# Kernel tuning notes

Hardware: AMD Instinct MI355X
Metric: run time of the kernel (lower is better)

The kernel has to match this reference:

```python
import jax, jax.numpy as jnp
import numpy as np

D_M, D_K, D_V, HEADS = 1024, 64, 64, 16
B, S = 2, 2048


def setup_inputs() -> dict:
    key = jax.random.key(0)
    ks = jax.random.split(key, 5)
    x = jax.random.normal(ks[0], (B, S, D_M), dtype=jnp.float32)
    # per-head projection weights (original deep-copies one rand init per head;
    # we give each head independent weights, matching the per-head param structure)
    Wk = jax.random.uniform(ks[1], (HEADS, D_M, D_K), dtype=jnp.float32)
    Wq = jax.random.uniform(ks[2], (HEADS, D_M, D_K), dtype=jnp.float32)
    Wv = jax.random.uniform(ks[3], (HEADS, D_M, D_V), dtype=jnp.float32)
    Wo = jax.random.uniform(ks[4], (HEADS * D_V, D_M), dtype=jnp.float32)
    return {"x": x, "Wk": Wk, "Wq": Wq, "Wv": Wv, "Wo": Wo}


def reference(x, Wk, Wq, Wv, Wo):
    # per-head QKV projections, batched over heads: [B,H,S,d]
    q = jnp.einsum("bsm,hmk->bhsk", x, Wq)
    k = jnp.einsum("bsm,hmk->bhsk", x, Wk)
    v = jnp.einsum("bsm,hmv->bhsv", x, Wv)
    scale = 1.0 / jnp.sqrt(jnp.asarray(q.shape[-1], dtype=q.dtype))
    scores = jnp.einsum("bhsk,bhtk->bhst", q, k) * scale  # [B,H,S,S]
    attn = jax.nn.softmax(scores, axis=-1)
    ctx = jnp.einsum("bhst,bhtv->bhsv", attn, v)  # [B,H,S,d_v]
    # concat heads -> [B,S,H*d_v], then output projection
    ctx = jnp.transpose(ctx, (0, 2, 1, 3)).reshape(x.shape[0], x.shape[1], -1)
    return jnp.einsum("bsc,cm->bsm", ctx, Wo)
```

## Files before the change

### kernel.cpp

```cpp
#include <hip/hip_runtime.h>
#include <hip/hip_bf16.h>
#include <stdint.h>

#define DM   1024
#define DKV  64
#define HEADS 16
#define BATCH 2
#define SEQ  2048
#define BS   (BATCH*SEQ)
#define BHD  (BATCH*HEADS)

typedef __attribute__((ext_vector_type(8))) short bf16x8;
typedef __attribute__((ext_vector_type(4))) short bf16x4;
typedef __attribute__((ext_vector_type(4))) float f32x4;

__device__ inline unsigned fb(float f) { union { float f; unsigned u; } v; v.f = f; return v.u; }

__device__ inline unsigned short bf16_rtn(float f) {
  unsigned u = fb(f);
  unsigned r = u + 0x7fffu + ((u >> 16) & 1u);
  return (unsigned short)(r >> 16);
}
__device__ inline float bf16_to_f(unsigned short h) {
  union { unsigned u; float f; } v; v.u = ((unsigned)h) << 16; return v.f;
}
__device__ inline void split_bf16(float x, unsigned short& hi, unsigned short& lo) {
  hi = bf16_rtn(x);
  lo = bf16_rtn(x - bf16_to_f(hi));
}
__device__ inline unsigned pack2_bf16(float lo_elem, float hi_elem) {
  return __builtin_amdgcn_perm(fb(hi_elem) + 0x8000u, fb(lo_elem) + 0x8000u, 0x07060302u);
}

__device__ inline float fast_exp2(float x) {
#if __has_builtin(__builtin_amdgcn_exp2f)
  return __builtin_amdgcn_exp2f(x);
#else
  return exp2f(x);
#endif
}

__device__ inline f32x4 mfma16x16x16_bf16(bf16x4 a, bf16x4 b, f32x4 c) {
#if __has_builtin(__builtin_amdgcn_mfma_f32_16x16x16bf16_1k)
  return __builtin_amdgcn_mfma_f32_16x16x16bf16_1k(a, b, c, 0, 0, 0);
#else
  asm volatile("v_mfma_f32_16x16x16_bf16 %0, %1, %2, %0" : "+v"(c) : "v"(a), "v"(b));
  return c;
#endif
}

__device__ inline void stage16(const unsigned short* g, unsigned short* lds_base, int lane) {
#if __has_builtin(__builtin_amdgcn_global_load_lds)
  __builtin_amdgcn_global_load_lds((__attribute__((address_space(1))) void*)(g),
                                   (__attribute__((address_space(3))) void*)(lds_base),
                                   16, 0, 0);
#else
  *(bf16x8*)(lds_base + lane * 8) = *(const bf16x8*)g;
#endif
}

__device__ inline int swz(int row, int chunk) {
  return row * 64 + (((chunk ^ (row & 7)) & 7) << 3);
}

__global__ void cvt_x_split(const float* __restrict__ x,
                            unsigned short* __restrict__ xh, unsigned short* __restrict__ xl) {
  int i = (blockIdx.x * 256 + threadIdx.x) * 8;
  bf16x8 oh, ol;
  #pragma unroll
  for (int j = 0; j < 8; ++j) {
    unsigned short hi, lo;
    split_bf16(x[i + j], hi, lo);
    oh[j] = (short)hi; ol[j] = (short)lo;
  }
  *(bf16x8*)(xh + i) = oh;
  *(bf16x8*)(xl + i) = ol;
}

__global__ void pack_qkv_split(const float* __restrict__ Wq, const float* __restrict__ Wk,
                               const float* __restrict__ Wv,
                               unsigned short* __restrict__ Wh, unsigned short* __restrict__ Wl) {
  __shared__ float tile[64][65];
  int bid = blockIdx.x;
  int p = bid >> 8, h = (bid >> 4) & 15, mt = bid & 15;
  const float* W = (p == 0) ? Wq : (p == 1) ? Wk : Wv;
  const float* src = W + (size_t)h * (DM * DKV);
  int t = threadIdx.x;
  int m0 = mt * 64;
  #pragma unroll
  for (int pass = 0; pass < 16; ++pass) {
    int row = pass * 4 + (t >> 6), col = t & 63;
    tile[row][col] = src[(size_t)(m0 + row) * DKV + col];
  }
  __syncthreads();
  int cbase = p * 1024 + h * 64;
  #pragma unroll
  for (int pass = 0; pass < 16; ++pass) {
    int krow = pass * 4 + (t >> 6), mcol = t & 63;
    unsigned short hi, lo;
    split_bf16(tile[mcol][krow], hi, lo);
    size_t idx = (size_t)(cbase + krow) * DM + m0 + mcol;
    Wh[idx] = hi; Wl[idx] = lo;
  }
}

__global__ void pack_wo(const float* __restrict__ Wo, unsigned short* __restrict__ WoT) {
  __shared__ float tile[64][65];
  int ib = blockIdx.x >> 4, jb = blockIdx.x & 15;
  int t = threadIdx.x;
  #pragma unroll
  for (int pass = 0; pass < 16; ++pass) {
    int row = pass * 4 + (t >> 6), col = t & 63;
    tile[row][col] = Wo[(size_t)(ib * 64 + row) * DM + jb * 64 + col];
  }
  __syncthreads();
  #pragma unroll
  for (int pass = 0; pass < 16; ++pass) {
    int a = pass * 4 + (t >> 6), b = t & 63;
    WoT[(size_t)(jb * 64 + a) * DM + ib * 64 + b] = bf16_rtn(tile[b][a]);
  }
}

__global__ __launch_bounds__(256, 2)
void gemm_qk(const unsigned short* __restrict__ Ah, const unsigned short* __restrict__ Al,
             const unsigned short* __restrict__ Bh, const unsigned short* __restrict__ Bl,
             unsigned short* __restrict__ Qh, unsigned short* __restrict__ Ql,
             unsigned short* __restrict__ Kh, unsigned short* __restrict__ Kl) {
  __shared__ unsigned short AsH[128 * 64], AsL[128 * 64];
  __shared__ unsigned short BsH[128 * 64], BsL[128 * 64];
  const int tid = threadIdx.x;
  const int w = tid >> 6, lane = tid & 63;
  const int quad = lane >> 4, l16 = lane & 15;
  const int wm = w >> 1, wn = w & 1;
  const int bn = blockIdx.x, bm = blockIdx.y;

  f32x4 acc[4][4];
  #pragma unroll
  for (int i = 0; i < 4; ++i)
    #pragma unroll
    for (int j = 0; j < 4; ++j) acc[i][j] = (f32x4){0.f, 0.f, 0.f, 0.f};

  const int r8 = lane >> 3, c8 = lane & 7;
  const int cs = c8 ^ r8;
  const size_t offA = (size_t)(bm * 128 + w * 32 + r8) * DM + cs * 8;
  const size_t offB = (size_t)(bn * 128 + w * 32 + r8) * DM + cs * 8;

  for (int kk = 0; kk < DM / 64; ++kk) {
    #pragma unroll
    for (int ps = 0; ps < 4; ++ps) {
      unsigned short* dA = AsH + (w * 32 + ps * 8) * 64;
      unsigned short* dAl = AsL + (w * 32 + ps * 8) * 64;
      unsigned short* dB = BsH + (w * 32 + ps * 8) * 64;
      unsigned short* dBl = BsL + (w * 32 + ps * 8) * 64;
      stage16(Ah + offA + kk * 64 + ps * 8 * DM, dA,  lane);
      stage16(Al + offA + kk * 64 + ps * 8 * DM, dAl, lane);
      stage16(Bh + offB + kk * 64 + ps * 8 * DM, dB,  lane);
      stage16(Bl + offB + kk * 64 + ps * 8 * DM, dBl, lane);
    }
    asm volatile("s_waitcnt vmcnt(0)" ::: "memory");
    __syncthreads();
    #pragma unroll
    for (int ks = 0; ks < 2; ++ks) {
      bf16x8 afh[4], afl[4], bfh[4], bfl[4];
      #pragma unroll
      for (int mt = 0; mt < 4; ++mt) {
        int row = wm * 64 + mt * 16 + l16;
        int ad = row * 64 + ((((ks * 4 + quad) ^ (row & 7)) & 7) << 3);
        afh[mt] = *(const bf16x8*)(AsH + ad);
        afl[mt] = *(const bf16x8*)(AsL + ad);
      }
      #pragma unroll
      for (int nt = 0; nt < 4; ++nt) {
        int row = wn * 64 + nt * 16 + l16;
        int ad = row * 64 + ((((ks * 4 + quad) ^ (row & 7)) & 7) << 3);
        bfh[nt] = *(const bf16x8*)(BsH + ad);
        bfl[nt] = *(const bf16x8*)(BsL + ad);
      }
      #pragma unroll
      for (int mt = 0; mt < 4; ++mt)
        #pragma unroll
        for (int nt = 0; nt < 4; ++nt) {
          acc[mt][nt] = __builtin_amdgcn_mfma_f32_16x16x32_bf16(afh[mt], bfh[nt], acc[mt][nt], 0, 0, 0);
          acc[mt][nt] = __builtin_amdgcn_mfma_f32_16x16x32_bf16(afh[mt], bfl[nt], acc[mt][nt], 0, 0, 0);
          acc[mt][nt] = __builtin_amdgcn_mfma_f32_16x16x32_bf16(afl[mt], bfh[nt], acc[mt][nt], 0, 0, 0);
        }
    }
    __syncthreads();
  }

  const float SCL = 0.18033688011112042f;
  #pragma unroll
  for (int mt = 0; mt < 4; ++mt) {
    int m_g = bm * 128 + wm * 64 + mt * 16 + quad * 4;
    #pragma unroll
    for (int nt = 0; nt < 4; ++nt) {
      int n_g = bn * 128 + wn * 64 + nt * 16 + l16;
      int p = n_g >> 10, h = (n_g >> 6) & 15, k = n_g & 63;
      #pragma unroll
      for (int r = 0; r < 4; ++r) {
        int row = m_g + r;
        int b = row >> 11, s = row & 2047;
        int bh = b * HEADS + h;
        float v = acc[mt][nt][r];
        size_t idx = ((size_t)(bh * SEQ + s)) * DKV + k;
        unsigned short hi, lo;
        if (p == 0) {
          split_bf16(v * SCL, hi, lo);
          Qh[idx] = hi; Ql[idx] = lo;
        } else {
          split_bf16(v, hi, lo);
          Kh[idx] = hi; Kl[idx] = lo;
        }
      }
    }
  }
}

__global__ __launch_bounds__(256, 2)
void gemm_v(const unsigned short* __restrict__ A, const unsigned short* __restrict__ Bt,
            unsigned short* __restrict__ Vt) {
  __shared__ unsigned short As[64 * 64];
  __shared__ unsigned short Bs[128 * 64];
  const int tid = threadIdx.x;
  const int w = tid >> 6, lane = tid & 63;
  const int quad = lane >> 4, l16 = lane & 15;
  const int wm = w >> 1, wn = w & 1;
  const int bn = blockIdx.x, bm = blockIdx.y;

  f32x4 acc[2][4];
  #pragma unroll
  for (int i = 0; i < 2; ++i)
    #pragma unroll
    for (int j = 0; j < 4; ++j) acc[i][j] = (f32x4){0.f, 0.f, 0.f, 0.f};

  const int r8 = lane >> 3, c8 = lane & 7;
  const int cs = c8 ^ r8;
  const size_t offA = (size_t)(bm * 64 + w * 16 + r8) * DM + cs * 8;
  const size_t offB = (size_t)(bn * 128 + w * 32 + r8) * DM + cs * 8;

  for (int kk = 0; kk < DM / 64; ++kk) {
    #pragma unroll
    for (int ps = 0; ps < 2; ++ps)
      stage16(A + offA + kk * 64 + ps * 8 * DM, As + (w * 16 + ps * 8) * 64, lane);
    #pragma unroll
    for (int ps = 0; ps < 4; ++ps)
      stage16(Bt + offB + kk * 64 + ps * 8 * DM, Bs + (w * 32 + ps * 8) * 64, lane);
    asm volatile("s_waitcnt vmcnt(0)" ::: "memory");
    __syncthreads();
    #pragma unroll
    for (int ks = 0; ks < 2; ++ks) {
      bf16x8 af[2], bfr[4];
      #pragma unroll
      for (int mt = 0; mt < 2; ++mt) {
        int row = wm * 32 + mt * 16 + l16;
        af[mt] = *(const bf16x8*)(As + row * 64 + ((((ks * 4 + quad) ^ (row & 7)) & 7) << 3));
      }
      #pragma unroll
      for (int nt = 0; nt < 4; ++nt) {
        int row = wn * 64 + nt * 16 + l16;
        bfr[nt] = *(const bf16x8*)(Bs + row * 64 + ((((ks * 4 + quad) ^ (row & 7)) & 7) << 3));
      }
      #pragma unroll
      for (int mt = 0; mt < 2; ++mt)
        #pragma unroll
        for (int nt = 0; nt < 4; ++nt)
          acc[mt][nt] = __builtin_amdgcn_mfma_f32_16x16x32_bf16(af[mt], bfr[nt], acc[mt][nt], 0, 0, 0);
    }
    __syncthreads();
  }

  #pragma unroll
  for (int mt = 0; mt < 2; ++mt) {
    int m_g = bm * 64 + wm * 32 + mt * 16 + quad * 4;
    #pragma unroll
    for (int nt = 0; nt < 4; ++nt) {
      int n_g = bn * 128 + wn * 64 + nt * 16 + l16;
      int h = n_g >> 6, k = n_g & 63;
      #pragma unroll
      for (int r = 0; r < 4; ++r) {
        int row = m_g + r;
        int b = row >> 11, s = row & 2047;
        int bh = b * HEADS + h;
        Vt[((size_t)(bh * DKV + k)) * SEQ + s] = bf16_rtn(acc[mt][nt][r]);
      }
    }
  }
}

__global__ __launch_bounds__(256, 2)
void flash(const unsigned short* __restrict__ Qh, const unsigned short* __restrict__ Ql,
           const unsigned short* __restrict__ Kh, const unsigned short* __restrict__ Kl,
           const unsigned short* __restrict__ Vt, unsigned short* __restrict__ ctx) {
  __shared__ unsigned short KtH[2][64 * 64], KtL[2][64 * 64], Vts[2][64 * 64];
  const int tid = threadIdx.x;
  const int w = tid >> 6, lane = tid & 63, quad = lane >> 4, l16 = lane & 15;
  const int bh = blockIdx.x;
  const int q0 = blockIdx.y * 128;

  bf16x8 qfh[2][2], qfl[2][2];
  #pragma unroll
  for (int qt = 0; qt < 2; ++qt) {
    int qrow = q0 + w * 32 + qt * 16 + l16;
    size_t base = ((size_t)(bh * SEQ + qrow)) * DKV + quad * 8;
    qfh[qt][0] = *(const bf16x8*)(Qh + base);
    qfh[qt][1] = *(const bf16x8*)(Qh + base + 32);
    qfl[qt][0] = *(const bf16x8*)(Ql + base);
    qfl[qt][1] = *(const bf16x8*)(Ql + base + 32);
  }

  float m_run[2] = {-1e30f, -1e30f};
  float l_run[2] = {0.f, 0.f};
  f32x4 acc[2][4];
  #pragma unroll
  for (int qt = 0; qt < 2; ++qt)
    #pragma unroll
    for (int vt = 0; vt < 4; ++vt) acc[qt][vt] = (f32x4){0.f, 0.f, 0.f, 0.f};

  const int srow = w * 16 + (lane >> 3);
  const int csrc = (lane & 7) ^ (lane >> 3);
  const unsigned short* kh_src = Kh + ((size_t)(bh * SEQ) + srow) * DKV + csrc * 8;
  const unsigned short* kl_src = Kl + ((size_t)(bh * SEQ) + srow) * DKV + csrc * 8;
  const unsigned short* v_src  = Vt + ((size_t)(bh * DKV) + srow) * SEQ + csrc * 8;

  #define STAGE_K(buf, kt0)                                                     \
    do {                                                                        \
      unsigned short* dH = &KtH[buf][(w * 16) * 64];                            \
      unsigned short* dL = &KtL[buf][(w * 16) * 64];                            \
      stage16(kh_src + (size_t)(kt0) * 64 * DKV,           dH,       lane);     \
      stage16(kh_src + (size_t)(kt0) * 64 * DKV + 8 * DKV, dH + 512, lane);     \
      stage16(kl_src + (size_t)(kt0) * 64 * DKV,           dL,       lane);     \
      stage16(kl_src + (size_t)(kt0) * 64 * DKV + 8 * DKV, dL + 512, lane);     \
    } while (0)
  #define STAGE_V(buf, kt0)                                                     \
    do {                                                                        \
      unsigned short* dV = &Vts[buf][(w * 16) * 64];                            \
      stage16(v_src + (kt0) * 64,           dV,       lane);                    \
      stage16(v_src + (kt0) * 64 + 8 * SEQ, dV + 512, lane);                    \
    } while (0)

  #define QK_HALF(STV, KHP, KLP, MT0)                                           \
    _Pragma("unroll")                                                           \
    for (int mt = (MT0); mt < (MT0) + 2; ++mt) {                                \
      int rowA = mt * 16 + l16;                                                 \
      bf16x8 kah0 = *(const bf16x8*)((KHP) + swz(rowA, quad));                  \
      bf16x8 kah1 = *(const bf16x8*)((KHP) + swz(rowA, quad + 4));              \
      bf16x8 kal0 = *(const bf16x8*)((KLP) + swz(rowA, quad));                  \
      bf16x8 kal1 = *(const bf16x8*)((KLP) + swz(rowA, quad + 4));              \
      _Pragma("unroll")                                                         \
      for (int qt = 0; qt < 2; ++qt) {                                          \
        f32x4 c = (f32x4){0.f, 0.f, 0.f, 0.f};                                  \
        c = __builtin_amdgcn_mfma_f32_16x16x32_bf16(kah0, qfh[qt][0], c, 0, 0, 0); \
        c = __builtin_amdgcn_mfma_f32_16x16x32_bf16(kah1, qfh[qt][1], c, 0, 0, 0); \
        c = __builtin_amdgcn_mfma_f32_16x16x32_bf16(kah0, qfl[qt][0], c, 0, 0, 0); \
        c = __builtin_amdgcn_mfma_f32_16x16x32_bf16(kah1, qfl[qt][1], c, 0, 0, 0); \
        c = __builtin_amdgcn_mfma_f32_16x16x32_bf16(kal0, qfh[qt][0], c, 0, 0, 0); \
        c = __builtin_amdgcn_mfma_f32_16x16x32_bf16(kal1, qfh[qt][1], c, 0, 0, 0); \
        (STV)[mt][qt] = c;                                                      \
      }                                                                         \
    }

  #define SM_QT(QT)                                                             \
    {                                                                           \
      float cm = -1e30f;                                                        \
      _Pragma("unroll")                                                         \
      for (int mt = 0; mt < 4; ++mt)                                            \
        _Pragma("unroll")                                                       \
        for (int r = 0; r < 4; ++r) cm = fmaxf(cm, st[mt][QT][r]);              \
      cm = fmaxf(cm, __shfl_xor(cm, 16));                                       \
      cm = fmaxf(cm, __shfl_xor(cm, 32));                                       \
      float mn = fmaxf(cm, m_run[QT]);                                          \
      float ssum = 0.f;                                                         \
      _Pragma("unroll")                                                         \
      for (int mt = 0; mt < 4; ++mt) {                                          \
        float p0 = fast_exp2(st[mt][QT][0] - mn);                               \
        float p1 = fast_exp2(st[mt][QT][1] - mn);                               \
        float p2 = fast_exp2(st[mt][QT][2] - mn);                               \
        float p3 = fast_exp2(st[mt][QT][3] - mn);                               \
        ssum += (p0 + p1) + (p2 + p3);                                          \
        union { bf16x4 v; unsigned u2[2]; } pk;                                 \
        pk.u2[0] = pack2_bf16(p0, p1);                                          \
        pk.u2[1] = pack2_bf16(p2, p3);                                          \
        pb[QT][mt] = pk.v;                                                      \
      }                                                                         \
      ssum += __shfl_xor(ssum, 16);                                             \
      ssum += __shfl_xor(ssum, 32);                                             \
      float alpha = fast_exp2(m_run[QT] - mn);                                  \
      m_run[QT] = mn;                                                           \
      l_run[QT] = l_run[QT] * alpha + ssum;                                     \
      _Pragma("unroll")                                                         \
      for (int vt = 0; vt < 4; ++vt) acc[QT][vt] = acc[QT][vt] * alpha;         \
    }

  #define PV_ALL(VSP)                                                           \
    _Pragma("unroll")                                                           \
    for (int vt = 0; vt < 4; ++vt)                                              \
      _Pragma("unroll")                                                         \
      for (int mt = 0; mt < 4; ++mt) {                                          \
        int row = vt * 16 + l16;                                                \
        int addr = row * 64 + ((((mt * 2 + (quad >> 1)) ^ (row & 7)) & 7) << 3) + (quad & 1) * 4; \
        bf16x4 va = *(const bf16x4*)((VSP) + addr);                             \
        _Pragma("unroll")                                                       \
        for (int qt = 0; qt < 2; ++qt)                                          \
          acc[qt][vt] = mfma16x16x16_bf16(va, pb[qt][mt], acc[qt][vt]);         \
      }

  STAGE_K(0, 0);
  STAGE_V(0, 0);
  STAGE_K(1, 1);
  asm volatile("s_waitcnt vmcnt(0)" ::: "memory");
  __syncthreads();

  f32x4 st[4][2];
  QK_HALF(st, KtH[0], KtL[0], 0);
  QK_HALF(st, KtH[0], KtL[0], 2);

  #pragma unroll 2
  for (int t = 0; t < SEQ / 64 - 1; ++t) {
    const int cb = t & 1, nb = (t + 1) & 1;
    if (t + 2 < SEQ / 64) STAGE_K(cb, t + 2);
    STAGE_V(nb, t + 1);

    const unsigned short* kHn = KtH[nb];
    const unsigned short* kLn = KtL[nb];
    const unsigned short* vS  = Vts[cb];

    bf16x4 pb[2][4];
    f32x4 stn[4][2];
    SM_QT(0);
    QK_HALF(stn, kHn, kLn, 0);
    SM_QT(1);
    QK_HALF(stn, kHn, kLn, 2);
    PV_ALL(vS);

    #pragma unroll
    for (int mt = 0; mt < 4; ++mt)
      #pragma unroll
      for (int qt = 0; qt < 2; ++qt) st[mt][qt] = stn[mt][qt];

    asm volatile("s_waitcnt vmcnt(0)" ::: "memory");
    __syncthreads();
  }

  {
    bf16x4 pb[2][4];
    SM_QT(0);
    SM_QT(1);
    PV_ALL(Vts[(SEQ / 64 - 1) & 1]);
  }
  #undef STAGE_K
  #undef STAGE_V
  #undef QK_HALF
  #undef SM_QT
  #undef PV_ALL

  int h = bh & 15, b = bh >> 4;
  #pragma unroll
  for (int qt = 0; qt < 2; ++qt) {
    float inv = 1.0f / l_run[qt];
    int bs = b * SEQ + q0 + w * 32 + qt * 16 + l16;
    #pragma unroll
    for (int vt = 0; vt < 4; ++vt) {
      union { bf16x4 v; unsigned u2[2]; } pk;
      pk.u2[0] = pack2_bf16(acc[qt][vt][0] * inv, acc[qt][vt][1] * inv);
      pk.u2[1] = pack2_bf16(acc[qt][vt][2] * inv, acc[qt][vt][3] * inv);
      *(bf16x4*)(ctx + (size_t)bs * DM + h * 64 + vt * 16 + quad * 4) = pk.v;
    }
  }
}

__global__ __launch_bounds__(256, 2)
void gemm_out(const unsigned short* __restrict__ A, const unsigned short* __restrict__ Bt,
              float* __restrict__ out) {
  __shared__ unsigned short As[64 * 64];
  __shared__ unsigned short Bs[128 * 64];
  const int tid = threadIdx.x;
  const int w = tid >> 6, lane = tid & 63;
  const int quad = lane >> 4, l16 = lane & 15;
  const int wm = w >> 1, wn = w & 1;
  const int bn = blockIdx.x, bm = blockIdx.y;

  f32x4 acc[2][4];
  #pragma unroll
  for (int i = 0; i < 2; ++i)
    #pragma unroll
    for (int j = 0; j < 4; ++j) acc[i][j] = (f32x4){0.f, 0.f, 0.f, 0.f};

  const int r8 = lane >> 3, c8 = lane & 7;
  const int cs = c8 ^ r8;
  const size_t offA = (size_t)(bm * 64 + w * 16 + r8) * DM + cs * 8;
  const size_t offB = (size_t)(bn * 128 + w * 32 + r8) * DM + cs * 8;

  for (int kk = 0; kk < DM / 64; ++kk) {
    #pragma unroll
    for (int ps = 0; ps < 2; ++ps)
      stage16(A + offA + kk * 64 + ps * 8 * DM, As + (w * 16 + ps * 8) * 64, lane);
    #pragma unroll
    for (int ps = 0; ps < 4; ++ps)
      stage16(Bt + offB + kk * 64 + ps * 8 * DM, Bs + (w * 32 + ps * 8) * 64, lane);
    asm volatile("s_waitcnt vmcnt(0)" ::: "memory");
    __syncthreads();
    #pragma unroll
    for (int ks = 0; ks < 2; ++ks) {
      bf16x8 af[2], bfr[4];
      #pragma unroll
      for (int mt = 0; mt < 2; ++mt) {
        int row = wm * 32 + mt * 16 + l16;
        af[mt] = *(const bf16x8*)(As + row * 64 + ((((ks * 4 + quad) ^ (row & 7)) & 7) << 3));
      }
      #pragma unroll
      for (int nt = 0; nt < 4; ++nt) {
        int row = wn * 64 + nt * 16 + l16;
        bfr[nt] = *(const bf16x8*)(Bs + row * 64 + ((((ks * 4 + quad) ^ (row & 7)) & 7) << 3));
      }
      #pragma unroll
      for (int mt = 0; mt < 2; ++mt)
        #pragma unroll
        for (int nt = 0; nt < 4; ++nt)
          acc[mt][nt] = __builtin_amdgcn_mfma_f32_16x16x32_bf16(af[mt], bfr[nt], acc[mt][nt], 0, 0, 0);
    }
    __syncthreads();
  }

  #pragma unroll
  for (int mt = 0; mt < 2; ++mt) {
    int m_g = bm * 64 + wm * 32 + mt * 16 + quad * 4;
    #pragma unroll
    for (int nt = 0; nt < 4; ++nt) {
      int n_g = bn * 128 + wn * 64 + nt * 16 + l16;
      #pragma unroll
      for (int r = 0; r < 4; ++r)
        out[(size_t)(m_g + r) * DM + n_g] = acc[mt][nt][r];
    }
  }
}

extern "C" void kernel_launch(void* const* d_in, const int* in_sizes, int n_in,
                              void* d_out, int out_size, void* d_ws, size_t ws_size,
                              hipStream_t stream) {
  const float* x  = (const float*)d_in[0];
  const float* Wk = (const float*)d_in[1];
  const float* Wq = (const float*)d_in[2];
  const float* Wv = (const float*)d_in[3];
  const float* Wo = (const float*)d_in[4];
  float* out = (float*)d_out;

  unsigned short* xh  = (unsigned short*)d_ws;
  unsigned short* xl  = xh  + (size_t)BS * DM;
  unsigned short* Wh  = xl  + (size_t)BS * DM;
  unsigned short* Wl  = Wh  + (size_t)3 * DM * DM;
  unsigned short* WoT = Wl  + (size_t)3 * DM * DM;
  unsigned short* Qh  = WoT + (size_t)DM * DM;
  unsigned short* Ql  = Qh  + (size_t)BHD * SEQ * DKV;
  unsigned short* Kh  = Ql  + (size_t)BHD * SEQ * DKV;
  unsigned short* Kl  = Kh  + (size_t)BHD * SEQ * DKV;
  unsigned short* Vtb = Kl  + (size_t)BHD * SEQ * DKV;
  unsigned short* ctx = Vtb + (size_t)BHD * SEQ * DKV;

  cvt_x_split<<<(BS * DM) / (256 * 8), 256, 0, stream>>>(x, xh, xl);
  pack_qkv_split<<<3 * 16 * 16, 256, 0, stream>>>(Wq, Wk, Wv, Wh, Wl);
  pack_wo<<<16 * 16, 256, 0, stream>>>(Wo, WoT);
  gemm_qk<<<dim3(16, 32), 256, 0, stream>>>(xh, xl, Wh, Wl, Qh, Ql, Kh, Kl);
  gemm_v<<<dim3(8, 64), 256, 0, stream>>>(xh, Wh + (size_t)2048 * DM, Vtb);
  flash<<<dim3(BHD, SEQ / 128), 256, 0, stream>>>(Qh, Ql, Kh, Kl, Vtb, ctx);
  gemm_out<<<dim3(8, 64), 256, 0, stream>>>(ctx, WoT, out);
}
```

Baseline: 251.7 us.

## Merge QK and V projection kernels, add lazy softmax rescale and MFMA priority

The separate QK and V projection GEMMs become one launch, with blocks 0–511 doing the split-precision QK work and blocks 512–1023 doing V from a shared LDS buffer, removing a launch and letting the two workloads overlap. In the flash kernel, the running max and rescale are only updated when some lane's local max exceeds the running max by more than 8. The cross-lane row-sum reduction moves to the epilogue. s_setprio is raised around the MFMA sections. The lazy threshold relies on exp2 values up to 2^8 staying safe in bf16/fp32, and the merged kernel now reserves the larger LDS footprint for every block.

```diff
diff --git a/kernel.cpp b/kernel.cpp
--- a/kernel.cpp
+++ b/kernel.cpp
@@ -122,166 +122,162 @@
 }
 
 __global__ __launch_bounds__(256, 2)
-void gemm_qk(const unsigned short* __restrict__ Ah, const unsigned short* __restrict__ Al,
-             const unsigned short* __restrict__ Bh, const unsigned short* __restrict__ Bl,
-             unsigned short* __restrict__ Qh, unsigned short* __restrict__ Ql,
-             unsigned short* __restrict__ Kh, unsigned short* __restrict__ Kl) {
-  __shared__ unsigned short AsH[128 * 64], AsL[128 * 64];
-  __shared__ unsigned short BsH[128 * 64], BsL[128 * 64];
+void gemm_qkv(const unsigned short* __restrict__ Ah, const unsigned short* __restrict__ Al,
+              const unsigned short* __restrict__ Bh, const unsigned short* __restrict__ Bl,
+              unsigned short* __restrict__ Qh, unsigned short* __restrict__ Ql,
+              unsigned short* __restrict__ Kh, unsigned short* __restrict__ Kl,
+              unsigned short* __restrict__ Vt) {
+  __shared__ unsigned short smem[32768];
   const int tid = threadIdx.x;
   const int w = tid >> 6, lane = tid & 63;
   const int quad = lane >> 4, l16 = lane & 15;
   const int wm = w >> 1, wn = w & 1;
-  const int bn = blockIdx.x, bm = blockIdx.y;
-
-  f32x4 acc[4][4];
-  #pragma unroll
-  for (int i = 0; i < 4; ++i)
-    #pragma unroll
-    for (int j = 0; j < 4; ++j) acc[i][j] = (f32x4){0.f, 0.f, 0.f, 0.f};
-
+  const int bid = blockIdx.x;
   const int r8 = lane >> 3, c8 = lane & 7;
   const int cs = c8 ^ r8;
-  const size_t offA = (size_t)(bm * 128 + w * 32 + r8) * DM + cs * 8;
-  const size_t offB = (size_t)(bn * 128 + w * 32 + r8) * DM + cs * 8;
-
-  for (int kk = 0; kk < DM / 64; ++kk) {
-    #pragma unroll
-    for (int ps = 0; ps < 4; ++ps) {
-      unsigned short* dA = AsH + (w * 32 + ps * 8) * 64;
-      unsigned short* dAl = AsL + (w * 32 + ps * 8) * 64;
-      unsigned short* dB = BsH + (w * 32 + ps * 8) * 64;
-      unsigned short* dBl = BsL + (w * 32 + ps * 8) * 64;
-      stage16(Ah + offA + kk * 64 + ps * 8 * DM, dA,  lane);
-      stage16(Al + offA + kk * 64 + ps * 8 * DM, dAl, lane);
-      stage16(Bh + offB + kk * 64 + ps * 8 * DM, dB,  lane);
-      stage16(Bl + offB + kk * 64 + ps * 8 * DM, dBl, lane);
-    }
-    asm volatile("s_waitcnt vmcnt(0)" ::: "memory");
-    __syncthreads();
-    #pragma unroll
-    for (int ks = 0; ks < 2; ++ks) {
-      bf16x8 afh[4], afl[4], bfh[4], bfl[4];
-      #pragma unroll
-      for (int mt = 0; mt < 4; ++mt) {
-        int row = wm * 64 + mt * 16 + l16;
-        int ad = row * 64 + ((((ks * 4 + quad) ^ (row & 7)) & 7) << 3);
-        afh[mt] = *(const bf16x8*)(AsH + ad);
-        afl[mt] = *(const bf16x8*)(AsL + ad);
-      }
+
+  if (bid < 512) {
+    unsigned short* AsH = smem;
+    unsigned short* AsL = smem + 8192;
+    unsigned short* BsH = smem + 16384;
+    unsigned short* BsL = smem + 24576;
+    const int bn = bid & 15, bm = bid >> 4;
+
+    f32x4 acc[4][4];
+    #pragma unroll
+    for (int i = 0; i < 4; ++i)
+      #pragma unroll
+      for (int j = 0; j < 4; ++j) acc[i][j] = (f32x4){0.f, 0.f, 0.f, 0.f};
+
+    const size_t offA = (size_t)(bm * 128 + w * 32 + r8) * DM + cs * 8;
+    const size_t offB = (size_t)(bn * 128 + w * 32 + r8) * DM + cs * 8;
+
+    for (int kk = 0; kk < DM / 64; ++kk) {
+      #pragma unroll
+      for (int ps = 0; ps < 4; ++ps) {
+        stage16(Ah + offA + kk * 64 + ps * 8 * DM, AsH + (w * 32 + ps * 8) * 64, lane);
+        stage16(Al + offA + kk * 64 + ps * 8 * DM, AsL + (w * 32 + ps * 8) * 64, lane);
+        stage16(Bh + offB + kk * 64 + ps * 8 * DM, BsH + (w * 32 + ps * 8) * 64, lane);
+        stage16(Bl + offB + kk * 64 + ps * 8 * DM, BsL + (w * 32 + ps * 8) * 64, lane);
+      }
+      asm volatile("s_waitcnt vmcnt(0)" ::: "memory");
+      __syncthreads();
+      #pragma unroll
+      for (int ks = 0; ks < 2; ++ks) {
+        bf16x8 afh[4], afl[4], bfh[4], bfl[4];
+        #pragma unroll
+        for (int mt = 0; mt < 4; ++mt) {
+          int row = wm * 64 + mt * 16 + l16;
+          int ad = row * 64 + ((((ks * 4 + quad) ^ (row & 7)) & 7) << 3);
+          afh[mt] = *(const bf16x8*)(AsH + ad);
+          afl[mt] = *(const bf16x8*)(AsL + ad);
+        }
+        #pragma unroll
+        for (int nt = 0; nt < 4; ++nt) {
+          int row = wn * 64 + nt * 16 + l16;
+          int ad = row * 64 + ((((ks * 4 + quad) ^ (row & 7)) & 7) << 3);
+          bfh[nt] = *(const bf16x8*)(BsH + ad);
+          bfl[nt] = *(const bf16x8*)(BsL + ad);
+        }
+        #pragma unroll
+        for (int mt = 0; mt < 4; ++mt)
+          #pragma unroll
+          for (int nt = 0; nt < 4; ++nt) {
+            acc[mt][nt] = __builtin_amdgcn_mfma_f32_16x16x32_bf16(afh[mt], bfh[nt], acc[mt][nt], 0, 0, 0);
+            acc[mt][nt] = __builtin_amdgcn_mfma_f32_16x16x32_bf16(afh[mt], bfl[nt], acc[mt][nt], 0, 0, 0);
+            acc[mt][nt] = __builtin_amdgcn_mfma_f32_16x16x32_bf16(afl[mt], bfh[nt], acc[mt][nt], 0, 0, 0);
+          }
+      }
+      __syncthreads();
+    }
+
+    const float SCL = 0.18033688011112042f;
+    #pragma unroll
+    for (int mt = 0; mt < 4; ++mt) {
+      int m_g = bm * 128 + wm * 64 + mt * 16 + quad * 4;
       #pragma unroll
       for (int nt = 0; nt < 4; ++nt) {
-        int row = wn * 64 + nt * 16 + l16;
-        int ad = row * 64 + ((((ks * 4 + quad) ^ (row & 7)) & 7) << 3);
-        bfh[nt] = *(const bf16x8*)(BsH + ad);
-        bfl[nt] = *(const bf16x8*)(BsL + ad);
-      }
-      #pragma unroll
-      for (int mt = 0; mt < 4; ++mt)
+        int n_g = bn * 128 + wn * 64 + nt * 16 + l16;
+        int p = n_g >> 10, h = (n_g >> 6) & 15, k = n_g & 63;
+        #pragma unroll
+        for (int r = 0; r < 4; ++r) {
+          int row = m_g + r;
+          int b = row >> 11, s = row & 2047;
+          int bh = b * HEADS + h;
+          float v = acc[mt][nt][r];
+          size_t idx = ((size_t)(bh * SEQ + s)) * DKV + k;
+          unsigned short hi, lo;
+          if (p == 0) {
+            split_bf16(v * SCL, hi, lo);
+            Qh[idx] = hi; Ql[idx] = lo;
+          } else {
+            split_bf16(v, hi, lo);
+            Kh[idx] = hi; Kl[idx] = lo;
+          }
+        }
+      }
+    }
+  } else {
+    unsigned short* As = smem;
+    unsigned short* Bs = smem + 4096;
+    const int vid = bid - 512;
+    const int bn = vid & 7, bm = vid >> 3;
+    const unsigned short* Bt = Bh + (size_t)2048 * DM;
+
+    f32x4 acc[2][4];
+    #pragma unroll
+    for (int i = 0; i < 2; ++i)
+      #pragma unroll
+      for (int j = 0; j < 4; ++j) acc[i][j] = (f32x4){0.f, 0.f, 0.f, 0.f};
+
+    const size_t offA = (size_t)(bm * 64 + w * 16 + r8) * DM + cs * 8;
+    const size_t offB = (size_t)(bn * 128 + w * 32 + r8) * DM + cs * 8;
+
+    for (int kk = 0; kk < DM / 64; ++kk) {
+      #pragma unroll
+      for (int ps = 0; ps < 2; ++ps)
+        stage16(Ah + offA + kk * 64 + ps * 8 * DM, As + (w * 16 + ps * 8) * 64, lane);
+      #pragma unroll
+      for (int ps = 0; ps < 4; ++ps)
+        stage16(Bt + offB + kk * 64 + ps * 8 * DM, Bs + (w * 32 + ps * 8) * 64, lane);
+      asm volatile("s_waitcnt vmcnt(0)" ::: "memory");
+      __syncthreads();
+      #pragma unroll
+      for (int ks = 0; ks < 2; ++ks) {
+        bf16x8 af[2], bfr[4];
+        #pragma unroll
+        for (int mt = 0; mt < 2; ++mt) {
+          int row = wm * 32 + mt * 16 + l16;
+          af[mt] = *(const bf16x8*)(As + row * 64 + ((((ks * 4 + quad) ^ (row & 7)) & 7) << 3));
+        }
         #pragma unroll
         for (int nt = 0; nt < 4; ++nt) {
-          acc[mt][nt] = __builtin_amdgcn_mfma_f32_16x16x32_bf16(afh[mt], bfh[nt], acc[mt][nt], 0, 0, 0);
-          acc[mt][nt] = __builtin_amdgcn_mfma_f32_16x16x32_bf16(afh[mt], bfl[nt], acc[mt][nt], 0, 0, 0);
-          acc[mt][nt] = __builtin_amdgcn_mfma_f32_16x16x32_bf16(afl[mt], bfh[nt], acc[mt][nt], 0, 0, 0);
+          int row = wn * 64 + nt * 16 + l16;
+          bfr[nt] = *(const bf16x8*)(Bs + row * 64 + ((((ks * 4 + quad) ^ (row & 7)) & 7) << 3));
         }
-    }
-    __syncthreads();
-  }
-
-  const float SCL = 0.18033688011112042f;
-  #pragma unroll
-  for (int mt = 0; mt < 4; ++mt) {
-    int m_g = bm * 128 + wm * 64 + mt * 16 + quad * 4;
-    #pragma unroll
-    for (int nt = 0; nt < 4; ++nt) {
-      int n_g = bn * 128 + wn * 64 + nt * 16 + l16;
-      int p = n_g >> 10, h = (n_g >> 6) & 15, k = n_g & 63;
-      #pragma unroll
-      for (int r = 0; r < 4; ++r) {
-        int row = m_g + r;
-        int b = row >> 11, s = row & 2047;
-        int bh = b * HEADS + h;
-        float v = acc[mt][nt][r];
-        size_t idx = ((size_t)(bh * SEQ + s)) * DKV + k;
-        unsigned short hi, lo;
-        if (p == 0) {
-          split_bf16(v * SCL, hi, lo);
-          Qh[idx] = hi; Ql[idx] = lo;
-        } else {
-          split_bf16(v, hi, lo);
-          Kh[idx] = hi; Kl[idx] = lo;
+        #pragma unroll
+        for (int mt = 0; mt < 2; ++mt)
+          #pragma unroll
+          for (int nt = 0; nt < 4; ++nt)
+            acc[mt][nt] = __builtin_amdgcn_mfma_f32_16x16x32_bf16(af[mt], bfr[nt], acc[mt][nt], 0, 0, 0);
+      }
+      __syncthreads();
+    }
+
+    #pragma unroll
+    for (int mt = 0; mt < 2; ++mt) {
+      int m_g = bm * 64 + wm * 32 + mt * 16 + quad * 4;
+      #pragma unroll
+      for (int nt = 0; nt < 4; ++nt) {
+        int n_g = bn * 128 + wn * 64 + nt * 16 + l16;
+        int h = n_g >> 6, k = n_g & 63;
+        #pragma unroll
+        for (int r = 0; r < 4; ++r) {
+          int row = m_g + r;
+          int b = row >> 11, s = row & 2047;
+          int bh = b * HEADS + h;
+          Vt[((size_t)(bh * DKV + k)) * SEQ + s] = bf16_rtn(acc[mt][nt][r]);
         }
-      }
-    }
-  }
-}
-
-__global__ __launch_bounds__(256, 2)
-void gemm_v(const unsigned short* __restrict__ A, const unsigned short* __restrict__ Bt,
-            unsigned short* __restrict__ Vt) {
-  __shared__ unsigned short As[64 * 64];
-  __shared__ unsigned short Bs[128 * 64];
-  const int tid = threadIdx.x;
-  const int w = tid >> 6, lane = tid & 63;
-  const int quad = lane >> 4, l16 = lane & 15;
-  const int wm = w >> 1, wn = w & 1;
-  const int bn = blockIdx.x, bm = blockIdx.y;
-
-  f32x4 acc[2][4];
-  #pragma unroll
-  for (int i = 0; i < 2; ++i)
-    #pragma unroll
-    for (int j = 0; j < 4; ++j) acc[i][j] = (f32x4){0.f, 0.f, 0.f, 0.f};
-
-  const int r8 = lane >> 3, c8 = lane & 7;
-  const int cs = c8 ^ r8;
-  const size_t offA = (size_t)(bm * 64 + w * 16 + r8) * DM + cs * 8;
-  const size_t offB = (size_t)(bn * 128 + w * 32 + r8) * DM + cs * 8;
-
-  for (int kk = 0; kk < DM / 64; ++kk) {
-    #pragma unroll
-    for (int ps = 0; ps < 2; ++ps)
-      stage16(A + offA + kk * 64 + ps * 8 * DM, As + (w * 16 + ps * 8) * 64, lane);
-    #pragma unroll
-    for (int ps = 0; ps < 4; ++ps)
-      stage16(Bt + offB + kk * 64 + ps * 8 * DM, Bs + (w * 32 + ps * 8) * 64, lane);
-    asm volatile("s_waitcnt vmcnt(0)" ::: "memory");
-    __syncthreads();
-    #pragma unroll
-    for (int ks = 0; ks < 2; ++ks) {
-      bf16x8 af[2], bfr[4];
-      #pragma unroll
-      for (int mt = 0; mt < 2; ++mt) {
-        int row = wm * 32 + mt * 16 + l16;
-        af[mt] = *(const bf16x8*)(As + row * 64 + ((((ks * 4 + quad) ^ (row & 7)) & 7) << 3));
-      }
-      #pragma unroll
-      for (int nt = 0; nt < 4; ++nt) {
-        int row = wn * 64 + nt * 16 + l16;
-        bfr[nt] = *(const bf16x8*)(Bs + row * 64 + ((((ks * 4 + quad) ^ (row & 7)) & 7) << 3));
-      }
-      #pragma unroll
-      for (int mt = 0; mt < 2; ++mt)
-        #pragma unroll
-        for (int nt = 0; nt < 4; ++nt)
-          acc[mt][nt] = __builtin_amdgcn_mfma_f32_16x16x32_bf16(af[mt], bfr[nt], acc[mt][nt], 0, 0, 0);
-    }
-    __syncthreads();
-  }
-
-  #pragma unroll
-  for (int mt = 0; mt < 2; ++mt) {
-    int m_g = bm * 64 + wm * 32 + mt * 16 + quad * 4;
-    #pragma unroll
-    for (int nt = 0; nt < 4; ++nt) {
-      int n_g = bn * 128 + wn * 64 + nt * 16 + l16;
-      int h = n_g >> 6, k = n_g & 63;
-      #pragma unroll
-      for (int r = 0; r < 4; ++r) {
-        int row = m_g + r;
-        int b = row >> 11, s = row & 2047;
-        int bh = b * HEADS + h;
-        Vt[((size_t)(bh * DKV + k)) * SEQ + s] = bf16_rtn(acc[mt][nt][r]);
       }
     }
   }
@@ -366,9 +362,17 @@
       for (int mt = 0; mt < 4; ++mt)                                            \
         _Pragma("unroll")                                                       \
         for (int r = 0; r < 4; ++r) cm = fmaxf(cm, st[mt][QT][r]);              \
-      cm = fmaxf(cm, __shfl_xor(cm, 16));                                       \
-      cm = fmaxf(cm, __shfl_xor(cm, 32));                                       \
-      float mn = fmaxf(cm, m_run[QT]);                                          \
+      if (!__all(cm <= m_run[QT] + 8.0f)) {                                     \
+        cm = fmaxf(cm, __shfl_xor(cm, 16));                                     \
+        cm = fmaxf(cm, __shfl_xor(cm, 32));                                     \
+        float mn = fmaxf(cm, m_run[QT]);                                        \
+        float alpha = fast_exp2(m_run[QT] - mn);                                \
+        m_run[QT] = mn;                                                         \
+        l_run[QT] *= alpha;                                                     \
+        _Pragma("unroll")                                                       \
+        for (int vt = 0; vt < 4; ++vt) acc[QT][vt] = acc[QT][vt] * alpha;       \
+      }                                                                         \
+      float mn = m_run[QT];                                                     \
       float ssum = 0.f;                                                         \
       _Pragma("unroll")                                                         \
       for (int mt = 0; mt < 4; ++mt) {                                          \
@@ -382,13 +386,7 @@
         pk.u2[1] = pack2_bf16(p2, p3);                                          \
         pb[QT][mt] = pk.v;                                                      \
       }                                                                         \
-      ssum += __shfl_xor(ssum, 16);                                             \
-      ssum += __shfl_xor(ssum, 32);                                             \
-      float alpha = fast_exp2(m_run[QT] - mn);                                  \
-      m_run[QT] = mn;                                                           \
-      l_run[QT] = l_run[QT] * alpha + ssum;                                     \
-      _Pragma("unroll")                                                         \
-      for (int vt = 0; vt < 4; ++vt) acc[QT][vt] = acc[QT][vt] * alpha;         \
+      l_run[QT] += ssum;                                                        \
     }
 
   #define PV_ALL(VSP)                                                           \
@@ -411,8 +409,10 @@
   __syncthreads();
 
   f32x4 st[4][2];
+  __builtin_amdgcn_s_setprio(1);
   QK_HALF(st, KtH[0], KtL[0], 0);
   QK_HALF(st, KtH[0], KtL[0], 2);
+  __builtin_amdgcn_s_setprio(0);
 
   #pragma unroll 2
   for (int t = 0; t < SEQ / 64 - 1; ++t) {
@@ -427,10 +427,14 @@
     bf16x4 pb[2][4];
     f32x4 stn[4][2];
     SM_QT(0);
+    __builtin_amdgcn_s_setprio(1);
     QK_HALF(stn, kHn, kLn, 0);
+    __builtin_amdgcn_s_setprio(0);
     SM_QT(1);
+    __builtin_amdgcn_s_setprio(1);
     QK_HALF(stn, kHn, kLn, 2);
     PV_ALL(vS);
+    __builtin_amdgcn_s_setprio(0);
 
     #pragma unroll
     for (int mt = 0; mt < 4; ++mt)
@@ -456,7 +460,10 @@
   int h = bh & 15, b = bh >> 4;
   #pragma unroll
   for (int qt = 0; qt < 2; ++qt) {
-    float inv = 1.0f / l_run[qt];
+    float lt = l_run[qt];
+    lt += __shfl_xor(lt, 16);
+    lt += __shfl_xor(lt, 32);
+    float inv = 1.0f / lt;
     int bs = b * SEQ + q0 + w * 32 + qt * 16 + l16;
     #pragma unroll
     for (int vt = 0; vt < 4; ++vt) {
@@ -559,8 +566,7 @@
   cvt_x_split<<<(BS * DM) / (256 * 8), 256, 0, stream>>>(x, xh, xl);
   pack_qkv_split<<<3 * 16 * 16, 256, 0, stream>>>(Wq, Wk, Wv, Wh, Wl);
   pack_wo<<<16 * 16, 256, 0, stream>>>(Wo, WoT);
-  gemm_qk<<<dim3(16, 32), 256, 0, stream>>>(xh, xl, Wh, Wl, Qh, Ql, Kh, Kl);
-  gemm_v<<<dim3(8, 64), 256, 0, stream>>>(xh, Wh + (size_t)2048 * DM, Vtb);
+  gemm_qkv<<<1024, 256, 0, stream>>>(xh, xl, Wh, Wl, Qh, Ql, Kh, Kl, Vtb);
   flash<<<dim3(BHD, SEQ / 128), 256, 0, stream>>>(Qh, Ql, Kh, Kl, Vtb, ctx);
   gemm_out<<<dim3(8, 64), 256, 0, stream>>>(ctx, WoT, out);
 }
```

Result: faster. 241.6 us (-4.0%).
